# Performance work log

Hardware: AMD Instinct MI355X
Metric: run time of the kernel (lower is better)

## Reference

```python
import math
import jax
import jax.numpy as jnp
from jax import lax
import numpy as np

SEQ = 1024   # must be a perfect square
BSZ = 16
D = 1024     # embed_dim
NDIM = 2
SIDE = 32    # sqrt(SEQ) == one_side_length
SCALE = float(np.sqrt(1.0 / NDIM))


def setup_inputs() -> dict:
    key = jax.random.key(0)
    ks = jax.random.split(key, 8)
    x = jax.random.normal(ks[0], (SEQ, BSZ, D), dtype=jnp.float32)
    A1 = 0.2 * jax.random.normal(ks[1], (D, NDIM), dtype=jnp.float32)
    A2 = 0.2 * jax.random.normal(ks[2], (D, NDIM), dtype=jnp.float32)
    B1 = 0.2 * jax.random.normal(ks[3], (D, NDIM), dtype=jnp.float32)
    B2 = 0.2 * jax.random.normal(ks[4], (D, NDIM), dtype=jnp.float32)
    C1 = jax.random.normal(ks[5], (D, NDIM), dtype=jnp.float32)
    C2 = jax.random.normal(ks[6], (D, NDIM), dtype=jnp.float32)
    omega = jax.random.normal(ks[7], (D,), dtype=jnp.float32)
    return {"x": x, "A1": A1, "A2": A2, "B1": B1, "B2": B2,
            "C1": C1, "C2": C2, "omega": omega}


def _compute_kernel(A1, A2, B1, B2, C1, C2, n):
    """2D SSM impulse-response kernel K: (D, n, n).

    Recurrence (same math the coeff-matrix path-sum in compute_x_matrix encodes,
    cf. one_step):
      h[i,j] = a1*h[i,j-1] + a2*v[i,j-1] + b1*x[i,j]
      v[i,j] = a2*h[i-1,j] + a1*v[i-1,j] + b2*x[i,j]
      K[i,j] = <h[i,j], C1*scale> + <v[i,j], C2*scale>
    driven by a unit impulse at (0,0).
    """
    a1 = jax.nn.sigmoid(A1) * 0.5
    a2 = jax.nn.sigmoid(A2) * 0.5
    b1 = jax.nn.sigmoid(B1) * 0.5
    b2 = jax.nn.sigmoid(B2) * 0.5

    x_img = jnp.zeros((n, n), dtype=A1.dtype).at[0, 0].set(1.0)

    def row_step(carry, x_row):
        h_prev, v_prev = carry                     # (n, D, N) each
        v_row = a2 * h_prev + a1 * v_prev + b2 * x_row[:, None, None]
        # h depends on v of the PREVIOUS column in the current row
        sv = jnp.concatenate([jnp.zeros_like(v_row[:1]), v_row[:-1]], axis=0)

        def col_step(h_left, inp):
            sv_j, x_j = inp
            h_j = a1 * h_left + a2 * sv_j + b1 * x_j
            return h_j, h_j

        _, h_row = lax.scan(col_step, jnp.zeros((D, NDIM), dtype=A1.dtype),
                            (sv, x_row))
        return (h_row, v_row), (h_row, v_row)

    init = (jnp.zeros((n, D, NDIM), dtype=A1.dtype),
            jnp.zeros((n, D, NDIM), dtype=A1.dtype))
    _, (H, V) = lax.scan(row_step, init, x_img)    # (n, n, D, N)

    K = (jnp.einsum('ijdn,dn->ijd', H, C1 * SCALE)
         + jnp.einsum('ijdn,dn->ijd', V, C2 * SCALE))
    return jnp.transpose(K, (2, 0, 1))             # (D, n, n)


def reference(x, A1, A2, B1, B2, C1, C2, omega):
    seq_len, bsz, embed_dim = x.shape
    n = int(math.isqrt(seq_len))
    residual = x * omega                            # (S, B, D)

    k = _compute_kernel(A1, A2, B1, B2, C1, C2, n)  # (D, n, n)

    xi = jnp.transpose(x, (1, 2, 0)).reshape(bsz, embed_dim, n, n)
    s = (2 * n, 2 * n)
    kf = jnp.fft.rfft2(k.astype(jnp.float32), s=s)           # (D, 2n, n+1)
    xf = jnp.fft.rfft2(xi.astype(jnp.float32), s=s)          # (B, D, 2n, n+1)
    out = jnp.fft.irfft2(xf * kf, s=s)[..., :n, :n]          # (B, D, n, n)
    out = out.astype(x.dtype).reshape(bsz, embed_dim, seq_len)
    out = jnp.transpose(out, (2, 0, 1))                      # (S, B, D)
    return jax.nn.silu(out + residual)
```

## Files before the change

### kernel.cpp

```cpp
#include <hip/hip_runtime.h>
#include <math.h>

#define BSZ  16
#define DIM  1024
#define DPB  16
#define THREADS 512
#define SSTRIDE 17
#define LDSF   17472
#define LDSB   (LDSF * 4)

__device__ __forceinline__ float sigmoidf_(float v) {
    return __builtin_amdgcn_rcpf(1.0f + __expf(-v));
}

extern __shared__ float xs[];

__global__ __launch_bounds__(THREADS, 1) void ssm2d_kernel(
    const float* __restrict__ x,
    const float* __restrict__ A1, const float* __restrict__ A2,
    const float* __restrict__ B1, const float* __restrict__ B2,
    const float* __restrict__ C1, const float* __restrict__ C2,
    const float* __restrict__ omega,
    float* __restrict__ out)
{
    const int bx = blockIdx.x;
    const int b  = bx >> 6;
    const int d0 = (bx & 63) * DPB;
    const int t  = threadIdx.x;

    const int lane = t & 63;
    const int wv   = t >> 6;
    const int dd   = 2 * wv + (lane >> 5);
    const int i    = lane & 31;
    const int d    = d0 + dd;

    const float2 fA1 = *reinterpret_cast<const float2*>(A1 + 2 * d);
    const float2 fA2 = *reinterpret_cast<const float2*>(A2 + 2 * d);
    const float2 fB1 = *reinterpret_cast<const float2*>(B1 + 2 * d);
    const float2 fB2 = *reinterpret_cast<const float2*>(B2 + 2 * d);
    const float2 fC1 = *reinterpret_cast<const float2*>(C1 + 2 * d);
    const float2 fC2 = *reinterpret_cast<const float2*>(C2 + 2 * d);
    const float  om  = omega[d];

    const float a1c0 = sigmoidf_(fA1.x) * 0.5f, a1c1 = sigmoidf_(fA1.y) * 0.5f;
    const float a2c0 = sigmoidf_(fA2.x) * 0.5f, a2c1 = sigmoidf_(fA2.y) * 0.5f;
    const float b1c0 = sigmoidf_(fB1.x) * 0.5f, b1c1 = sigmoidf_(fB1.y) * 0.5f;
    const float b2c0 = sigmoidf_(fB2.x) * 0.5f, b2c1 = sigmoidf_(fB2.y) * 0.5f;
    const float sc   = 0.70710678118654752f;
    const float c1s0 = fC1.x * sc, c1s1 = fC1.y * sc;
    const float c2s0 = fC2.x * sc, c2s1 = fC2.y * sc;
    const float a1z0 = (i == 0) ? 0.f : a1c0, a1z1 = (i == 0) ? 0.f : a1c1;
    const float a2z0 = (i == 0) ? 0.f : a2c0, a2z1 = (i == 0) ? 0.f : a2c1;

    const float* xb = x + (size_t)b * DIM + d0;
    float4 L[8];
    #pragma unroll
    for (int k = 0; k < 8; ++k) {
        const int g = t + k * THREADS;
        const int s = g >> 2;
        const int q = g & 3;
        L[k] = *reinterpret_cast<const float4*>(
            xb + (size_t)s * (BSZ * DIM) + 4 * q);
    }
    #pragma unroll
    for (int k = 0; k < 8; ++k) {
        const int g = t + k * THREADS;
        const int s = g >> 2;
        const int q = g & 3;
        float* p = xs + SSTRIDE * s + 4 * q;
        p[0] = L[k].x; p[1] = L[k].y; p[2] = L[k].z; p[3] = L[k].w;
    }

    __syncthreads();

    float* rp = xs + 527 * i + dd;

    float h0 = 0.f, h1 = 0.f, v0 = 0.f, v1 = 0.f;
    float xq0 = rp[0 * SSTRIDE];
    float xq1 = rp[1 * SSTRIDE];
    float xq2 = rp[2 * SSTRIDE];

#define SSTEP(TS, XQ) do {                                                   \
        const bool  valid = ((unsigned)((TS) - i) < 32u);                    \
        const float xv    = valid ? (XQ) : 0.f;                              \
        const float t10 = b1c0 * xv, t11 = b1c1 * xv;                        \
        const float hn0 = fmaf(a1c0, h0, fmaf(a2c0, v0, t10));               \
        const float hn1 = fmaf(a1c1, h1, fmaf(a2c1, v1, t11));               \
        float vn0 = b2c0 * xv, vn1 = b2c1 * xv;                              \
        asm("s_nop 1\n\t"                                                    \
            "v_fmac_f32_dpp %0, %2, %6 wave_shr:1 row_mask:0xf bank_mask:0xf bound_ctrl:0\n\t" \
            "v_fmac_f32_dpp %1, %3, %7 wave_shr:1 row_mask:0xf bank_mask:0xf bound_ctrl:0\n\t" \
            "v_fmac_f32_dpp %0, %4, %8 wave_shr:1 row_mask:0xf bank_mask:0xf bound_ctrl:0\n\t" \
            "v_fmac_f32_dpp %1, %5, %9 wave_shr:1 row_mask:0xf bank_mask:0xf bound_ctrl:0"     \
            : "+v"(vn0), "+v"(vn1)                                           \
            : "v"(h0), "v"(h1), "v"(v0), "v"(v1),                            \
              "v"(a2z0), "v"(a2z1), "v"(a1z0), "v"(a1z1));                   \
        float y = hn0 * c1s0;                                                \
        y = fmaf(hn1, c1s1, y);                                              \
        y = fmaf(vn0, c2s0, y);                                              \
        y = fmaf(vn1, c2s1, y);                                              \
        const float z = fmaf(xv, om, y);                                     \
        const float o = z * sigmoidf_(z);                                    \
        if (valid) rp[SSTRIDE * (TS)] = o;                                   \
        h0 = hn0; h1 = hn1; v0 = vn0; v1 = vn1;                              \
    } while (0)

    #pragma unroll
    for (int ts = 0; ts < 63; ts += 3) {
        SSTEP(ts + 0, xq0); xq0 = rp[SSTRIDE * (ts + 3)];
        SSTEP(ts + 1, xq1); xq1 = rp[SSTRIDE * (ts + 4)];
        SSTEP(ts + 2, xq2); xq2 = rp[SSTRIDE * (ts + 5)];
    }
#undef SSTEP

    __syncthreads();

    float* ob = out + (size_t)b * DIM + d0;
    #pragma unroll
    for (int k = 0; k < 8; ++k) {
        const int g = t + k * THREADS;
        const int s = g >> 2;
        const int q = g & 3;
        const float* p = xs + SSTRIDE * s + 4 * q;
        float4 v;
        v.x = p[0]; v.y = p[1]; v.z = p[2]; v.w = p[3];
        *reinterpret_cast<float4*>(ob + (size_t)s * (BSZ * DIM) + 4 * q) = v;
    }
}

extern "C" void kernel_launch(void* const* d_in, const int* in_sizes, int n_in,
                              void* d_out, int out_size, void* d_ws, size_t ws_size,
                              hipStream_t stream) {
    const float* x     = (const float*)d_in[0];
    const float* A1    = (const float*)d_in[1];
    const float* A2    = (const float*)d_in[2];
    const float* B1    = (const float*)d_in[3];
    const float* B2    = (const float*)d_in[4];
    const float* C1    = (const float*)d_in[5];
    const float* C2    = (const float*)d_in[6];
    const float* omega = (const float*)d_in[7];
    float* out = (float*)d_out;

    (void)hipFuncSetAttribute(reinterpret_cast<const void*>(ssm2d_kernel),
                              hipFuncAttributeMaxDynamicSharedMemorySize, LDSB);

    dim3 grid(BSZ * (DIM / DPB));
    dim3 block(THREADS);
    hipLaunchKernelGGL(ssm2d_kernel, grid, block, LDSB, stream,
                       x, A1, A2, B1, B2, C1, C2, omega, out);
}
```

Before: 45.30 us.

## Process two batches per block and prefetch second batch during compute

Each block now handles two batch entries (b0 and b0+8) with the grid halved to 512 blocks. The global loads for the second batch are issued before the first compute pass, so their latency overlaps with the recurrence. Parameter setup and sigmoid evaluation are amortized across two batches. In exchange, the number of blocks drops, which may underfill CUs, and extra barriers are added.

Measured after the change: 47.13 us. +4.1%, slower.

```diff
diff --git a/kernel.cpp b/kernel.cpp
--- a/kernel.cpp
+++ b/kernel.cpp
@@ -24,7 +24,7 @@
     float* __restrict__ out)
 {
     const int bx = blockIdx.x;
-    const int b  = bx >> 6;
+    const int b0 = bx >> 6;
     const int d0 = (bx & 63) * DPB;
     const int t  = threadIdx.x;
 
@@ -52,33 +52,30 @@
     const float a1z0 = (i == 0) ? 0.f : a1c0, a1z1 = (i == 0) ? 0.f : a1c1;
     const float a2z0 = (i == 0) ? 0.f : a2c0, a2z1 = (i == 0) ? 0.f : a2c1;
 
-    const float* xb = x + (size_t)b * DIM + d0;
+    const int sbase_f = (t >> 2) * (BSZ * DIM) + (t & 3) * 4 + d0;
+    const int lds_t   = SSTRIDE * (t >> 2) + (t & 3) * 4;
+
     float4 L[8];
-    #pragma unroll
-    for (int k = 0; k < 8; ++k) {
-        const int g = t + k * THREADS;
-        const int s = g >> 2;
-        const int q = g & 3;
-        L[k] = *reinterpret_cast<const float4*>(
-            xb + (size_t)s * (BSZ * DIM) + 4 * q);
-    }
-    #pragma unroll
-    for (int k = 0; k < 8; ++k) {
-        const int g = t + k * THREADS;
-        const int s = g >> 2;
-        const int q = g & 3;
-        float* p = xs + SSTRIDE * s + 4 * q;
-        p[0] = L[k].x; p[1] = L[k].y; p[2] = L[k].z; p[3] = L[k].w;
-    }
 
-    __syncthreads();
+#define LOADT(B) {                                                           \
+        const float* gp = x + (size_t)sbase_f + (size_t)(B) * DIM;           \
+        _Pragma("unroll") for (int k = 0; k < 8; ++k)                        \
+            L[k] = *reinterpret_cast<const float4*>(                         \
+                gp + (size_t)k * (128 * BSZ * DIM)); }
+
+#define WRITELDS() {                                                         \
+        _Pragma("unroll") for (int k = 0; k < 8; ++k) {                      \
+            float* p = xs + lds_t + k * (128 * SSTRIDE);                     \
+            p[0]=L[k].x; p[1]=L[k].y; p[2]=L[k].z; p[3]=L[k].w; } }
+
+#define DRAINT(B) {                                                          \
+        float* op = out + (size_t)sbase_f + (size_t)(B) * DIM;               \
+        _Pragma("unroll") for (int k = 0; k < 8; ++k) {                      \
+            const float* p = xs + lds_t + k * (128 * SSTRIDE);               \
+            float4 v; v.x=p[0]; v.y=p[1]; v.z=p[2]; v.w=p[3];                \
+            *reinterpret_cast<float4*>(op + (size_t)k * (128 * BSZ * DIM)) = v; } }
 
     float* rp = xs + 527 * i + dd;
-
-    float h0 = 0.f, h1 = 0.f, v0 = 0.f, v1 = 0.f;
-    float xq0 = rp[0 * SSTRIDE];
-    float xq1 = rp[1 * SSTRIDE];
-    float xq2 = rp[2 * SSTRIDE];
 
 #define SSTEP(TS, XQ) do {                                                   \
         const bool  valid = ((unsigned)((TS) - i) < 32u);                    \
@@ -105,27 +102,36 @@
         h0 = hn0; h1 = hn1; v0 = vn0; v1 = vn1;                              \
     } while (0)
 
-    #pragma unroll
-    for (int ts = 0; ts < 63; ts += 3) {
-        SSTEP(ts + 0, xq0); xq0 = rp[SSTRIDE * (ts + 3)];
-        SSTEP(ts + 1, xq1); xq1 = rp[SSTRIDE * (ts + 4)];
-        SSTEP(ts + 2, xq2); xq2 = rp[SSTRIDE * (ts + 5)];
-    }
+#define COMPUTE() {                                                          \
+        float h0 = 0.f, h1 = 0.f, v0 = 0.f, v1 = 0.f;                        \
+        float xq0 = rp[0 * SSTRIDE];                                         \
+        float xq1 = rp[1 * SSTRIDE];                                         \
+        float xq2 = rp[2 * SSTRIDE];                                         \
+        _Pragma("unroll") for (int ts = 0; ts < 63; ts += 3) {               \
+            SSTEP(ts + 0, xq0); xq0 = rp[SSTRIDE * (ts + 3)];                \
+            SSTEP(ts + 1, xq1); xq1 = rp[SSTRIDE * (ts + 4)];                \
+            SSTEP(ts + 2, xq2); xq2 = rp[SSTRIDE * (ts + 5)];                \
+        } }
+
+    LOADT(b0);
+    WRITELDS();
+    LOADT(b0 + 8);
+    __syncthreads();
+    COMPUTE();
+    __syncthreads();
+    DRAINT(b0);
+    __syncthreads();
+    WRITELDS();
+    __syncthreads();
+    COMPUTE();
+    __syncthreads();
+    DRAINT(b0 + 8);
+
 #undef SSTEP
-
-    __syncthreads();
-
-    float* ob = out + (size_t)b * DIM + d0;
-    #pragma unroll
-    for (int k = 0; k < 8; ++k) {
-        const int g = t + k * THREADS;
-        const int s = g >> 2;
-        const int q = g & 3;
-        const float* p = xs + SSTRIDE * s + 4 * q;
-        float4 v;
-        v.x = p[0]; v.y = p[1]; v.z = p[2]; v.w = p[3];
-        *reinterpret_cast<float4*>(ob + (size_t)s * (BSZ * DIM) + 4 * q) = v;
-    }
+#undef COMPUTE
+#undef LOADT
+#undef WRITELDS
+#undef DRAINT
 }
 
 extern "C" void kernel_launch(void* const* d_in, const int* in_sizes, int n_in,
@@ -144,7 +150,7 @@
     (void)hipFuncSetAttribute(reinterpret_cast<const void*>(ssm2d_kernel),
                               hipFuncAttributeMaxDynamicSharedMemorySize, LDSB);
 
-    dim3 grid(BSZ * (DIM / DPB));
+    dim3 grid(512);
     dim3 block(THREADS);
     hipLaunchKernelGGL(ssm2d_kernel, grid, block, LDSB, stream,
                        x, A1, A2, B1, B2, C1, C2, omega, out);
```

## Warp-specialize blocks: compute waves scan while loader waves double-buffer next tile

Applied to the files above, without the earlier changes.

Each block now handles four batch tiles instead of one, with 1024 threads split into 512 compute threads running the diagonal scan and 512 producer threads that prefetch the next tile from global memory and write back the previous tile's output. LDS is double-buffered so loads and stores overlap with the scan, and the grid shrinks from 1024 to 256 blocks. This targets the serialized load, compute and store phases of each block, at the cost of fewer blocks, double the LDS per block and an extra barrier per tile.

Result: faster. 40.58 us (-10.4%).

```diff
diff --git a/kernel.cpp b/kernel.cpp
--- a/kernel.cpp
+++ b/kernel.cpp
@@ -4,10 +4,11 @@
 #define BSZ  16
 #define DIM  1024
 #define DPB  16
-#define THREADS 512
+#define THREADS 1024
+#define TPB  4
 #define SSTRIDE 17
-#define LDSF   17472
-#define LDSB   (LDSF * 4)
+#define BUFF 17472
+#define LDSB (2 * BUFF * 4)
 
 __device__ __forceinline__ float sigmoidf_(float v) {
     return __builtin_amdgcn_rcpf(1.0f + __expf(-v));
@@ -24,61 +25,56 @@
     float* __restrict__ out)
 {
     const int bx = blockIdx.x;
-    const int b  = bx >> 6;
+    const int bq = bx >> 6;
     const int d0 = (bx & 63) * DPB;
     const int t  = threadIdx.x;
 
     const int lane = t & 63;
     const int wv   = t >> 6;
-    const int dd   = 2 * wv + (lane >> 5);
     const int i    = lane & 31;
-    const int d    = d0 + dd;
 
-    const float2 fA1 = *reinterpret_cast<const float2*>(A1 + 2 * d);
-    const float2 fA2 = *reinterpret_cast<const float2*>(A2 + 2 * d);
-    const float2 fB1 = *reinterpret_cast<const float2*>(B1 + 2 * d);
-    const float2 fB2 = *reinterpret_cast<const float2*>(B2 + 2 * d);
-    const float2 fC1 = *reinterpret_cast<const float2*>(C1 + 2 * d);
-    const float2 fC2 = *reinterpret_cast<const float2*>(C2 + 2 * d);
-    const float  om  = omega[d];
-
-    const float a1c0 = sigmoidf_(fA1.x) * 0.5f, a1c1 = sigmoidf_(fA1.y) * 0.5f;
-    const float a2c0 = sigmoidf_(fA2.x) * 0.5f, a2c1 = sigmoidf_(fA2.y) * 0.5f;
-    const float b1c0 = sigmoidf_(fB1.x) * 0.5f, b1c1 = sigmoidf_(fB1.y) * 0.5f;
-    const float b2c0 = sigmoidf_(fB2.x) * 0.5f, b2c1 = sigmoidf_(fB2.y) * 0.5f;
-    const float sc   = 0.70710678118654752f;
-    const float c1s0 = fC1.x * sc, c1s1 = fC1.y * sc;
-    const float c2s0 = fC2.x * sc, c2s1 = fC2.y * sc;
-    const float a1z0 = (i == 0) ? 0.f : a1c0, a1z1 = (i == 0) ? 0.f : a1c1;
-    const float a2z0 = (i == 0) ? 0.f : a2c0, a2z1 = (i == 0) ? 0.f : a2c1;
-
-    const float* xb = x + (size_t)b * DIM + d0;
-    float4 L[8];
-    #pragma unroll
-    for (int k = 0; k < 8; ++k) {
-        const int g = t + k * THREADS;
-        const int s = g >> 2;
-        const int q = g & 3;
-        L[k] = *reinterpret_cast<const float4*>(
-            xb + (size_t)s * (BSZ * DIM) + 4 * q);
-    }
-    #pragma unroll
-    for (int k = 0; k < 8; ++k) {
-        const int g = t + k * THREADS;
-        const int s = g >> 2;
-        const int q = g & 3;
-        float* p = xs + SSTRIDE * s + 4 * q;
-        p[0] = L[k].x; p[1] = L[k].y; p[2] = L[k].z; p[3] = L[k].w;
+    float a1c0, a1c1, a2c0, a2c1, b1c0, b1c1, b2c0, b2c1;
+    float c1s0, c1s1, c2s0, c2s1, om;
+    float a1z0, a1z1, a2z0, a2z1;
+    int dd = 0;
+    if (t < 512) {
+        dd = 2 * wv + (lane >> 5);
+        const int d = d0 + dd;
+        const float2 fA1 = *reinterpret_cast<const float2*>(A1 + 2 * d);
+        const float2 fA2 = *reinterpret_cast<const float2*>(A2 + 2 * d);
+        const float2 fB1 = *reinterpret_cast<const float2*>(B1 + 2 * d);
+        const float2 fB2 = *reinterpret_cast<const float2*>(B2 + 2 * d);
+        const float2 fC1 = *reinterpret_cast<const float2*>(C1 + 2 * d);
+        const float2 fC2 = *reinterpret_cast<const float2*>(C2 + 2 * d);
+        om   = omega[d];
+        a1c0 = sigmoidf_(fA1.x) * 0.5f;  a1c1 = sigmoidf_(fA1.y) * 0.5f;
+        a2c0 = sigmoidf_(fA2.x) * 0.5f;  a2c1 = sigmoidf_(fA2.y) * 0.5f;
+        b1c0 = sigmoidf_(fB1.x) * 0.5f;  b1c1 = sigmoidf_(fB1.y) * 0.5f;
+        b2c0 = sigmoidf_(fB2.x) * 0.5f;  b2c1 = sigmoidf_(fB2.y) * 0.5f;
+        const float sc = 0.70710678118654752f;
+        c1s0 = fC1.x * sc;  c1s1 = fC1.y * sc;
+        c2s0 = fC2.x * sc;  c2s1 = fC2.y * sc;
+        a1z0 = (i == 0) ? 0.f : a1c0;  a1z1 = (i == 0) ? 0.f : a1c1;
+        a2z0 = (i == 0) ? 0.f : a2c0;  a2z1 = (i == 0) ? 0.f : a2c1;
     }
 
+    {
+        const int   srow  = t >> 2;
+        const int   qq    = (t & 3) * 4;
+        const float* gp = x + (size_t)srow * (BSZ * DIM)
+                            + (size_t)(4 * bq) * DIM + d0 + qq;
+        float4 P[4];
+        #pragma unroll
+        for (int k2 = 0; k2 < 4; ++k2)
+            P[k2] = *reinterpret_cast<const float4*>(
+                gp + (size_t)k2 * (256 * BSZ * DIM));
+        #pragma unroll
+        for (int k2 = 0; k2 < 4; ++k2) {
+            float* p = xs + SSTRIDE * (srow + 256 * k2) + qq;
+            p[0] = P[k2].x; p[1] = P[k2].y; p[2] = P[k2].z; p[3] = P[k2].w;
+        }
+    }
     __syncthreads();
-
-    float* rp = xs + 527 * i + dd;
-
-    float h0 = 0.f, h1 = 0.f, v0 = 0.f, v1 = 0.f;
-    float xq0 = rp[0 * SSTRIDE];
-    float xq1 = rp[1 * SSTRIDE];
-    float xq2 = rp[2 * SSTRIDE];
 
 #define SSTEP(TS, XQ) do {                                                   \
         const bool  valid = ((unsigned)((TS) - i) < 32u);                    \
@@ -105,26 +101,72 @@
         h0 = hn0; h1 = hn1; v0 = vn0; v1 = vn1;                              \
     } while (0)
 
-    #pragma unroll
-    for (int ts = 0; ts < 63; ts += 3) {
-        SSTEP(ts + 0, xq0); xq0 = rp[SSTRIDE * (ts + 3)];
-        SSTEP(ts + 1, xq1); xq1 = rp[SSTRIDE * (ts + 4)];
-        SSTEP(ts + 2, xq2); xq2 = rp[SSTRIDE * (ts + 5)];
+    #pragma unroll 1
+    for (int k = 0; k < TPB; ++k) {
+        float* bufC = xs + (k & 1) * BUFF;
+        float* bufO = xs + ((k + 1) & 1) * BUFF;
+
+        if (t < 512) {
+            float* rp = bufC + 527 * i + dd;
+            float h0 = 0.f, h1 = 0.f, v0 = 0.f, v1 = 0.f;
+            float xq0 = rp[0 * SSTRIDE];
+            float xq1 = rp[1 * SSTRIDE];
+            float xq2 = rp[2 * SSTRIDE];
+            #pragma unroll
+            for (int ts = 0; ts < 63; ts += 3) {
+                SSTEP(ts + 0, xq0); xq0 = rp[SSTRIDE * (ts + 3)];
+                SSTEP(ts + 1, xq1); xq1 = rp[SSTRIDE * (ts + 4)];
+                SSTEP(ts + 2, xq2); xq2 = rp[SSTRIDE * (ts + 5)];
+            }
+        } else {
+            const int   m    = t - 512;
+            const int   srow = m >> 2;
+            const int   qq   = (m & 3) * 4;
+            const size_t gb  = (size_t)srow * (BSZ * DIM) + d0 + qq;
+
+            float4 L[8];
+            if (k < TPB - 1) {
+                const float* gp = x + gb + (size_t)(4 * bq + k + 1) * DIM;
+                #pragma unroll
+                for (int k2 = 0; k2 < 8; ++k2)
+                    L[k2] = *reinterpret_cast<const float4*>(
+                        gp + (size_t)k2 * (128 * BSZ * DIM));
+            }
+            if (k > 0) {
+                float* op = out + gb + (size_t)(4 * bq + k - 1) * DIM;
+                #pragma unroll
+                for (int k2 = 0; k2 < 8; ++k2) {
+                    const float* p = bufO + SSTRIDE * (srow + 128 * k2) + qq;
+                    float4 v; v.x = p[0]; v.y = p[1]; v.z = p[2]; v.w = p[3];
+                    *reinterpret_cast<float4*>(
+                        op + (size_t)k2 * (128 * BSZ * DIM)) = v;
+                }
+            }
+            if (k < TPB - 1) {
+                #pragma unroll
+                for (int k2 = 0; k2 < 8; ++k2) {
+                    float* p = bufO + SSTRIDE * (srow + 128 * k2) + qq;
+                    p[0] = L[k2].x; p[1] = L[k2].y;
+                    p[2] = L[k2].z; p[3] = L[k2].w;
+                }
+            }
+        }
+        __syncthreads();
     }
 #undef SSTEP
 
-    __syncthreads();
-
-    float* ob = out + (size_t)b * DIM + d0;
-    #pragma unroll
-    for (int k = 0; k < 8; ++k) {
-        const int g = t + k * THREADS;
-        const int s = g >> 2;
-        const int q = g & 3;
-        const float* p = xs + SSTRIDE * s + 4 * q;
-        float4 v;
-        v.x = p[0]; v.y = p[1]; v.z = p[2]; v.w = p[3];
-        *reinterpret_cast<float4*>(ob + (size_t)s * (BSZ * DIM) + 4 * q) = v;
+    {
+        const int   srow = t >> 2;
+        const int   qq   = (t & 3) * 4;
+        const float* bufE = xs + ((TPB - 1) & 1) * BUFF;
+        float* op = out + (size_t)srow * (BSZ * DIM)
+                        + (size_t)(4 * bq + TPB - 1) * DIM + d0 + qq;
+        #pragma unroll
+        for (int k2 = 0; k2 < 4; ++k2) {
+            const float* p = bufE + SSTRIDE * (srow + 256 * k2) + qq;
+            float4 v; v.x = p[0]; v.y = p[1]; v.z = p[2]; v.w = p[3];
+            *reinterpret_cast<float4*>(op + (size_t)k2 * (256 * BSZ * DIM)) = v;
+        }
     }
 }
 
@@ -144,7 +186,7 @@
     (void)hipFuncSetAttribute(reinterpret_cast<const void*>(ssm2d_kernel),
                               hipFuncAttributeMaxDynamicSharedMemorySize, LDSB);
 
-    dim3 grid(BSZ * (DIM / DPB));
+    dim3 grid(256);
     dim3 block(THREADS);
     hipLaunchKernelGGL(ssm2d_kernel, grid, block, LDSB, stream,
                        x, A1, A2, B1, B2, C1, C2, omega, out);
```

## Double channels per block to 32 and split wavefront scan into pre/post phases

Applied to the files above, without the earlier changes.

Each block now covers 32 channels with 1024 threads, which halves the grid to 512 blocks and makes each sequence row a 128-byte contiguous load and store. The 63-step diagonal scan is split into a fill phase and a drain phase, so each phase uses a simpler validity test and drops the unsigned range check. __syncthreads is replaced by an explicit lgkmcnt wait plus s_barrier. Each block needs about 136KB of LDS and 1024 threads, which limits occupancy to one block per CU, and the 512 blocks may leave part of the machine idle.

New measurement: 46.53 us. +2.7%, slower.

```diff
diff --git a/kernel.cpp b/kernel.cpp
--- a/kernel.cpp
+++ b/kernel.cpp
@@ -3,14 +3,20 @@
 
 #define BSZ  16
 #define DIM  1024
-#define DPB  16
-#define THREADS 512
-#define SSTRIDE 17
-#define LDSF   17472
-#define LDSB   (LDSF * 4)
+#define DPB  32
+#define THREADS 1024
+#define SSTRIDE 33
+#define BUFF 34048
+#define LDSB (BUFF * 4)
 
 __device__ __forceinline__ float sigmoidf_(float v) {
     return __builtin_amdgcn_rcpf(1.0f + __expf(-v));
+}
+
+__device__ __forceinline__ void soft_barrier() {
+    asm volatile("s_waitcnt lgkmcnt(0)" ::: "memory");
+    __builtin_amdgcn_s_barrier();
+    asm volatile("" ::: "memory");
 }
 
 extern __shared__ float xs[];
@@ -23,15 +29,16 @@
     const float* __restrict__ omega,
     float* __restrict__ out)
 {
-    const int bx = blockIdx.x;
-    const int b  = bx >> 6;
-    const int d0 = (bx & 63) * DPB;
-    const int t  = threadIdx.x;
+    const int lx   = blockIdx.x;
+    const int dgrp = lx & 31;
+    const int b    = lx >> 5;
+    const int d0   = dgrp * DPB;
+    const int t    = threadIdx.x;
 
     const int lane = t & 63;
     const int wv   = t >> 6;
+    const int i    = lane & 31;
     const int dd   = 2 * wv + (lane >> 5);
-    const int i    = lane & 31;
     const int d    = d0 + dd;
 
     const float2 fA1 = *reinterpret_cast<const float2*>(A1 + 2 * d);
@@ -52,37 +59,28 @@
     const float a1z0 = (i == 0) ? 0.f : a1c0, a1z1 = (i == 0) ? 0.f : a1c1;
     const float a2z0 = (i == 0) ? 0.f : a2c0, a2z1 = (i == 0) ? 0.f : a2c1;
 
-    const float* xb = x + (size_t)b * DIM + d0;
-    float4 L[8];
-    #pragma unroll
-    for (int k = 0; k < 8; ++k) {
-        const int g = t + k * THREADS;
-        const int s = g >> 2;
-        const int q = g & 3;
-        L[k] = *reinterpret_cast<const float4*>(
-            xb + (size_t)s * (BSZ * DIM) + 4 * q);
+    const int  srow0 = t >> 3;
+    const int  qq    = (t & 7) * 4;
+    const size_t gb  = (size_t)srow0 * (BSZ * DIM) + (size_t)b * DIM + d0 + qq;
+
+    {
+        float4 P[8];
+        #pragma unroll
+        for (int k2 = 0; k2 < 8; ++k2)
+            P[k2] = *reinterpret_cast<const float4*>(
+                x + gb + (size_t)k2 * (128 * BSZ * DIM));
+        #pragma unroll
+        for (int k2 = 0; k2 < 8; ++k2) {
+            float* p = xs + SSTRIDE * (srow0 + 128 * k2) + qq;
+            p[0] = P[k2].x; p[1] = P[k2].y; p[2] = P[k2].z; p[3] = P[k2].w;
+        }
     }
-    #pragma unroll
-    for (int k = 0; k < 8; ++k) {
-        const int g = t + k * THREADS;
-        const int s = g >> 2;
-        const int q = g & 3;
-        float* p = xs + SSTRIDE * s + 4 * q;
-        p[0] = L[k].x; p[1] = L[k].y; p[2] = L[k].z; p[3] = L[k].w;
-    }
+    soft_barrier();
 
-    __syncthreads();
+    float* rp = xs + 1023 * i + dd;
 
-    float* rp = xs + 527 * i + dd;
-
-    float h0 = 0.f, h1 = 0.f, v0 = 0.f, v1 = 0.f;
-    float xq0 = rp[0 * SSTRIDE];
-    float xq1 = rp[1 * SSTRIDE];
-    float xq2 = rp[2 * SSTRIDE];
-
-#define SSTEP(TS, XQ) do {                                                   \
-        const bool  valid = ((unsigned)((TS) - i) < 32u);                    \
-        const float xv    = valid ? (XQ) : 0.f;                              \
+#define SBODY(XV_EXPR)                                                       \
+        const float xv = (XV_EXPR);                                          \
         const float t10 = b1c0 * xv, t11 = b1c1 * xv;                        \
         const float hn0 = fmaf(a1c0, h0, fmaf(a2c0, v0, t10));               \
         const float hn1 = fmaf(a1c1, h1, fmaf(a2c1, v1, t11));               \
@@ -100,31 +98,49 @@
         y = fmaf(vn0, c2s0, y);                                              \
         y = fmaf(vn1, c2s1, y);                                              \
         const float z = fmaf(xv, om, y);                                     \
-        const float o = z * sigmoidf_(z);                                    \
-        if (valid) rp[SSTRIDE * (TS)] = o;                                   \
-        h0 = hn0; h1 = hn1; v0 = vn0; v1 = vn1;                              \
-    } while (0)
+        const float o = z * sigmoidf_(z);
 
-    #pragma unroll
-    for (int ts = 0; ts < 63; ts += 3) {
-        SSTEP(ts + 0, xq0); xq0 = rp[SSTRIDE * (ts + 3)];
-        SSTEP(ts + 1, xq1); xq1 = rp[SSTRIDE * (ts + 4)];
-        SSTEP(ts + 2, xq2); xq2 = rp[SSTRIDE * (ts + 5)];
+#define SSTEP_PRE(TS, XQ) do {                                               \
+        const bool val = (i <= (TS));                                        \
+        SBODY(val ? (XQ) : 0.f)                                              \
+        if (val) rp[SSTRIDE * (TS)] = o;                                     \
+        h0 = hn0; h1 = hn1; v0 = vn0; v1 = vn1; } while (0)
+
+#define SSTEP_POST(TS, XQ) do { SBODY(XQ)                                    \
+        if (i >= (TS) - 31) rp[SSTRIDE * (TS)] = o;                          \
+        h0 = hn0; h1 = hn1; v0 = vn0; v1 = vn1; } while (0)
+
+    {
+        float h0 = 0.f, h1 = 0.f, v0 = 0.f, v1 = 0.f;
+        float xq0 = rp[0 * SSTRIDE];
+        float xq1 = rp[1 * SSTRIDE];
+        float xq2 = rp[2 * SSTRIDE];
+        #pragma unroll
+        for (int ts = 0; ts < 30; ts += 3) {
+            SSTEP_PRE(ts + 0, xq0); xq0 = rp[SSTRIDE * (ts + 3)];
+            SSTEP_PRE(ts + 1, xq1); xq1 = rp[SSTRIDE * (ts + 4)];
+            SSTEP_PRE(ts + 2, xq2); xq2 = rp[SSTRIDE * (ts + 5)];
+        }
+        SSTEP_PRE(30, xq0); xq0 = rp[SSTRIDE * 33];
+        #pragma unroll
+        for (int ts = 31; ts < 61; ts += 3) {
+            SSTEP_POST(ts + 0, xq1); xq1 = rp[SSTRIDE * (ts + 3)];
+            SSTEP_POST(ts + 1, xq2); xq2 = rp[SSTRIDE * (ts + 4)];
+            SSTEP_POST(ts + 2, xq0); xq0 = rp[SSTRIDE * (ts + 5)];
+        }
+        SSTEP_POST(61, xq1);
+        SSTEP_POST(62, xq2);
     }
-#undef SSTEP
+    soft_barrier();
 
-    __syncthreads();
-
-    float* ob = out + (size_t)b * DIM + d0;
-    #pragma unroll
-    for (int k = 0; k < 8; ++k) {
-        const int g = t + k * THREADS;
-        const int s = g >> 2;
-        const int q = g & 3;
-        const float* p = xs + SSTRIDE * s + 4 * q;
-        float4 v;
-        v.x = p[0]; v.y = p[1]; v.z = p[2]; v.w = p[3];
-        *reinterpret_cast<float4*>(ob + (size_t)s * (BSZ * DIM) + 4 * q) = v;
+    {
+        #pragma unroll
+        for (int k2 = 0; k2 < 8; ++k2) {
+            const float* p = xs + SSTRIDE * (srow0 + 128 * k2) + qq;
+            float4 v; v.x = p[0]; v.y = p[1]; v.z = p[2]; v.w = p[3];
+            *reinterpret_cast<float4*>(
+                out + gb + (size_t)k2 * (128 * BSZ * DIM)) = v;
+        }
     }
 }
 
@@ -144,7 +160,7 @@
     (void)hipFuncSetAttribute(reinterpret_cast<const void*>(ssm2d_kernel),
                               hipFuncAttributeMaxDynamicSharedMemorySize, LDSB);
 
-    dim3 grid(BSZ * (DIM / DPB));
+    dim3 grid(512);
     dim3 block(THREADS);
     hipLaunchKernelGGL(ssm2d_kernel, grid, block, LDSB, stream,
                        x, A1, A2, B1, B2, C1, C2, omega, out);
```
